# Optimization experiments

Hardware: AMD Instinct MI355X
Metric: run time of the kernel (lower is better)

The kernel has to match this reference:

```python
import jax, jax.numpy as jnp
import numpy as np
import math

BLOCK = 8
N_COEFF = BLOCK * BLOCK  # 64
N_SAMPLE = 250
SEED = 0  # args.seed

# zigzag order: flat index m*8+n from the hardcoded loc table
ZIGZAG = jnp.array([
    0, 1, 8, 16, 9, 2, 3, 10, 17, 24, 32, 25, 18, 11, 4, 5,
    12, 19, 26, 33, 40, 48, 41, 34, 27, 20, 13, 6, 7, 14, 21, 28,
    35, 42, 49, 56, 57, 50, 43, 36, 29, 22, 15, 23, 30, 37, 44, 51,
    58, 59, 52, 45, 38, 31, 39, 46, 53, 60, 61, 54, 47, 55, 62, 63
], dtype=jnp.int32)


def dct_matrix():
    Q = np.zeros((BLOCK, BLOCK), dtype=np.float32)
    Q[0, :] = math.sqrt(1.0 / BLOCK)
    for i in range(1, BLOCK):
        for j in range(BLOCK):
            Q[i, j] = math.sqrt(2.0 / BLOCK) * math.cos((2 * j + 1) * math.pi * i / (2.0 * BLOCK))
    return jnp.asarray(Q)


def setup_inputs() -> dict:
    key = jax.random.key(0)
    x = jax.random.uniform(key, (64, 3, 512, 512), dtype=jnp.float32)
    return {"x": x}


def reference(x):
    Q = dct_matrix()
    # rgb -> ycbcr, luminance channel only (module discards Cb/Cr)
    x255 = x * 255.0
    y = (0.299 * x255[:, 0] + 0.587 * x255[:, 1] + 0.114 * x255[:, 2]) / 255.0  # [B,H,W]
    B, H, W = y.shape
    a, b = H // BLOCK, W // BLOCK
    # split into 8x8 blocks: [B, a, b, 8, 8]
    blocks = y.reshape(B, a, BLOCK, b, BLOCK).transpose(0, 1, 3, 2, 4)
    # per-block 2D DCT: Q @ block @ Q^T, batched as one einsum
    dct = jnp.einsum('ij,nabjk,lk->nabil', Q, blocks, Q)  # [B,a,b,8,8]
    image_dct_result = dct.transpose(0, 1, 3, 2, 4).reshape(B, 1, H, W)
    # zigzag gather over flattened block coefficients -> [B, 64, a*b]
    dist = dct.reshape(B, a * b, N_COEFF)[:, :, ZIGZAG].transpose(0, 2, 1)
    # per (sample, coefficient) random permutation sampling of 250 blocks
    keys = jax.random.split(jax.random.key(SEED), B * N_COEFF)
    idx = jax.vmap(lambda k: jax.random.permutation(k, a * b)[:N_SAMPLE])(keys)
    idx = idx.reshape(B, N_COEFF, N_SAMPLE)
    dct_coeff_sample = jnp.take_along_axis(dist, idx, axis=2)  # [B,64,250]
    return image_dct_result, dct_coeff_sample
```

## Files before the change

kernel.cpp:

```cpp
#include <hip/hip_runtime.h>
#include <hip/hip_bf16.h>
#include <cstdint>


#define BATCH 64
#define HW 512
#define NBLK 4096
#define NSAMPLE 250
#define IMG_ELEMS (HW * HW)

#define A0 0.35355339059327373f
#define A1 0.49039264020161522f
#define A2 0.46193976625564337f
#define A3 0.41573480615127262f
#define A4 0.35355339059327379f
#define A5 0.27778511650980111f
#define A6 0.19134171618254492f
#define A7 0.09754516100806412f

__constant__ float Qc[8][8] = {
    { A0,  A0,  A0,  A0,  A0,  A0,  A0,  A0},
    { A1,  A3,  A5,  A7, -A7, -A5, -A3, -A1},
    { A2,  A6, -A6, -A2, -A2, -A6,  A6,  A2},
    { A3, -A7, -A1, -A5,  A5,  A1,  A7, -A3},
    { A4, -A4, -A4,  A4,  A4, -A4, -A4,  A4},
    { A5, -A1,  A7,  A3, -A3, -A7,  A1, -A5},
    { A6, -A2,  A2, -A6, -A6,  A2, -A2,  A6},
    { A7, -A5,  A3, -A1,  A1, -A3,  A5, -A7},
};

__constant__ int ZIGZAG[64] = {
    0, 1, 8, 16, 9, 2, 3, 10, 17, 24, 32, 25, 18, 11, 4, 5,
    12, 19, 26, 33, 40, 48, 41, 34, 27, 20, 13, 6, 7, 14, 21, 28,
    35, 42, 49, 56, 57, 50, 43, 36, 29, 22, 15, 23, 30, 37, 44, 51,
    58, 59, 52, 45, 38, 31, 39, 46, 53, 60, 61, 54, 47, 55, 62, 63
};

__device__ __forceinline__ uint32_t rotl32(uint32_t v, int d) {
    return (v << d) | (v >> (32 - d));
}

__device__ __forceinline__ void tf2x32(uint32_t k0, uint32_t k1,
                                       uint32_t x0, uint32_t x1,
                                       uint32_t& o0, uint32_t& o1) {
    uint32_t ks0 = k0, ks1 = k1, ks2 = k0 ^ k1 ^ 0x1BD11BDAu;
    x0 += ks0; x1 += ks1;
#define TF_R(r) { x0 += x1; x1 = rotl32(x1, r); x1 ^= x0; }
    TF_R(13) TF_R(15) TF_R(26) TF_R(6)
    x0 += ks1; x1 += ks2 + 1u;
    TF_R(17) TF_R(29) TF_R(16) TF_R(24)
    x0 += ks2; x1 += ks0 + 2u;
    TF_R(13) TF_R(15) TF_R(26) TF_R(6)
    x0 += ks0; x1 += ks1 + 3u;
    TF_R(17) TF_R(29) TF_R(16) TF_R(24)
    x0 += ks1; x1 += ks2 + 4u;
    TF_R(13) TF_R(15) TF_R(26) TF_R(6)
    x0 += ks2; x1 += ks0 + 5u;
#undef TF_R
    o0 = x0; o1 = x1;
}

__device__ __forceinline__ void build4096(
    uint32_t s0, uint32_t s1,
    uint32_t* __restrict__ pack32, uint32_t* __restrict__ hist,
    int tid, int w, int lane, uint32_t* __restrict__ wsum) {

    __syncthreads();
    ((uint4*)hist)[tid] = make_uint4(0u, 0u, 0u, 0u);
    ((uint4*)hist)[tid + 512] = make_uint4(0u, 0u, 0u, 0u);
    uint32_t keys[8];
#pragma unroll
    for (int e = 0; e < 8; ++e) {
        uint32_t o0, o1;
        tf2x32(s0, s1, 0u, (uint32_t)(tid + e * 512), o0, o1);
        keys[e] = o0 ^ o1;
    }
    __syncthreads();

    uint32_t ord[8];
#pragma unroll
    for (int e = 0; e < 8; ++e)
        ord[e] = atomicAdd(&hist[keys[e] >> 20], 1u);
    __syncthreads();

    uint4 va = ((const uint4*)hist)[tid * 2];
    uint4 vb = ((const uint4*)hist)[tid * 2 + 1];
    uint32_t ssum = va.x + va.y + va.z + va.w + vb.x + vb.y + vb.z + vb.w;
    uint32_t sc = ssum;
#pragma unroll
    for (int off = 1; off < 64; off <<= 1) {
        uint32_t t = __shfl_up(sc, off);
        if (lane >= off) sc += t;
    }
    if (lane == 63) wsum[w] = sc;
    __syncthreads();
    uint32_t ex = sc - ssum;
    for (int ww = 0; ww < w; ++ww) ex += wsum[ww];
    uint32_t p1 = ex + va.x, p2 = p1 + va.y, p3 = p2 + va.z, p4 = p3 + va.w;
    uint32_t p5 = p4 + vb.x, p6 = p5 + vb.y, p7 = p6 + vb.z, p8 = p7 + vb.w;
    ((uint4*)hist)[tid * 2] = make_uint4(p1, p2, p3, p4);
    ((uint4*)hist)[tid * 2 + 1] = make_uint4(p5, p6, p7, p8);
    __syncthreads();

#pragma unroll
    for (int e = 0; e < 8; ++e) {
        uint32_t bkt = keys[e] >> 20;
        uint32_t start = bkt ? hist[bkt - 1] : 0u;
        pack32[start + ord[e]] =
            ((keys[e] & 0xFFFFFu) << 12) | (uint32_t)(tid + e * 512);
    }
}

__device__ __forceinline__ uint32_t select4096(
    const uint32_t* __restrict__ hist, const uint32_t* __restrict__ pack32,
    uint32_t s) {
    uint32_t lo = 0, hi = 4095;
#pragma unroll
    for (int it = 0; it < 12; ++it) {
        uint32_t mid = (lo + hi) >> 1;
        if (hist[mid] > s) hi = mid; else lo = mid + 1;
    }
    uint32_t b = lo;
    uint32_t start = b ? hist[b - 1] : 0u;
    uint32_t L = hist[b] - start;
    uint32_t c = pack32[start];
    if (L > 1) {
        uint32_t k = s - start;
        for (uint32_t cand = 0; cand < L; ++cand) {
            uint32_t cc = pack32[start + cand];
            uint32_t cnt = 0;
            for (uint32_t o = 0; o < L; ++o)
                cnt += (pack32[start + o] < cc) ? 1u : 0u;
            if (cnt == k) { c = cc; break; }
        }
    }
    return c & 0xFFFu;
}

__global__ __launch_bounds__(512, 8) void fused_kernel(
    const float* __restrict__ x, float* __restrict__ out,
    uint32_t* __restrict__ ws) {
    __shared__ __align__(16) uint8_t smem[33280];
    __shared__ uint32_t wsum[8];

    const int tid = threadIdx.x;
    const int gb = blockIdx.x;

    {
        float* ylds = (float*)smem;
        const int b = gb >> 6;
        const int ai = gb & 63;
        const int row0 = ai * 8;
        const int h = tid >> 8;
        const int t2 = tid & 255;
        const int colbase = h * 256;

        {
            const int k = t2 >> 5;
            const int cg = t2 & 31;
            size_t off = (size_t)b * 3 * IMG_ELEMS + (size_t)(row0 + k) * HW +
                         colbase + cg * 8;
            float4 r0 = *(const float4*)(x + off);
            float4 r1 = *(const float4*)(x + off + 4);
            float4 g0 = *(const float4*)(x + off + IMG_ELEMS);
            float4 g1 = *(const float4*)(x + off + IMG_ELEMS + 4);
            float4 b0 = *(const float4*)(x + off + 2 * IMG_ELEMS);
            float4 b1 = *(const float4*)(x + off + 2 * IMG_ELEMS + 4);
            float R[8] = {r0.x, r0.y, r0.z, r0.w, r1.x, r1.y, r1.z, r1.w};
            float G[8] = {g0.x, g0.y, g0.z, g0.w, g1.x, g1.y, g1.z, g1.w};
            float B[8] = {b0.x, b0.y, b0.z, b0.w, b1.x, b1.y, b1.z, b1.w};
            float* yh = ylds + h * 2048 + k * 256;
#pragma unroll
            for (int jj = 0; jj < 8; ++jj) {
                float y = (0.299f * (R[jj] * 255.0f) + 0.587f * (G[jj] * 255.0f) +
                           0.114f * (B[jj] * 255.0f)) / 255.0f;
                yh[jj * 32 + cg] = y;
            }
        }
        __syncthreads();

        {
            const int i = t2 >> 5;
            const int bi = t2 & 31;
            const float* yh = ylds + h * 2048;
            float qrow[8];
#pragma unroll
            for (int k = 0; k < 8; ++k) qrow[k] = Qc[i][k];

            float acc[8];
#pragma unroll
            for (int j = 0; j < 8; ++j) acc[j] = 0.0f;
#pragma unroll
            for (int k = 0; k < 8; ++k) {
#pragma unroll
                for (int j = 0; j < 8; ++j)
                    acc[j] += qrow[k] * yh[k * 256 + j * 32 + bi];
            }

            float d[8];
#pragma unroll
            for (int j = 0; j < 8; ++j) {
                float s = 0.0f;
#pragma unroll
                for (int k = 0; k < 8; ++k) s += acc[k] * Qc[j][k];
                d[j] = s;
            }
            float4* o = (float4*)(out + (size_t)b * IMG_ELEMS +
                                  (size_t)(row0 + i) * HW + colbase + bi * 8);
            o[0] = make_float4(d[0], d[1], d[2], d[3]);
            o[1] = make_float4(d[4], d[5], d[6], d[7]);
        }
    }

    {
        uint32_t* pack32 = (uint32_t*)smem;
        uint32_t* hist = (uint32_t*)(smem + 16384);
        uint16_t* jsel = (uint16_t*)(smem + 32768);

        const int w = tid >> 6;
        const int lane = tid & 63;

        uint32_t k0, k1, n0, n1, sA0, sA1, sB0, sB1;
        tf2x32(0u, 0u, 0u, (uint32_t)gb, k0, k1);
        tf2x32(k0, k1, 0u, 0u, n0, n1);
        tf2x32(k0, k1, 0u, 1u, sA0, sA1);
        tf2x32(n0, n1, 0u, 1u, sB0, sB1);

        build4096(sB0, sB1, pack32, hist, tid, w, lane, wsum);
        __syncthreads();
        if (tid < NSAMPLE)
            jsel[tid] = (uint16_t)select4096(hist, pack32, (uint32_t)tid);

        build4096(sA0, sA1, pack32, hist, tid, w, lane, wsum);
        __syncthreads();

        int b = gb >> 6, c = gb & 63;
        int z = ZIGZAG[c];
        int i0z = z >> 3, j0z = z & 7;
        if (tid < NSAMPLE) {
            uint32_t i = select4096(hist, pack32, (uint32_t)jsel[tid]);
            int ai = (int)i >> 6, bi = (int)i & 63;
            ws[(size_t)gb * 256 + tid] =
                (uint32_t)((size_t)b * IMG_ELEMS +
                           (size_t)(ai * 8 + i0z) * HW + (bi * 8 + j0z));
        }
    }
}

__global__ __launch_bounds__(256) void gather_kernel(
    const float* __restrict__ img, const uint32_t* __restrict__ ws,
    float* __restrict__ out2) {
    const int gb = blockIdx.x;
    const int s = threadIdx.x;
    if (s < NSAMPLE)
        out2[(size_t)gb * NSAMPLE + s] = img[ws[(size_t)gb * 256 + s]];
}

extern "C" void kernel_launch(void* const* d_in, const int* in_sizes, int n_in,
                              void* d_out, int out_size, void* d_ws, size_t ws_size,
                              hipStream_t stream) {
    const float* x = (const float*)d_in[0];
    float* out = (float*)d_out;
    uint32_t* ws = (uint32_t*)d_ws;
    fused_kernel<<<NBLK, 512, 0, stream>>>(x, out, ws);
    gather_kernel<<<BATCH * 64, 256, 0, stream>>>(
        out, ws, out + (size_t)BATCH * IMG_ELEMS);
}
```

Before: 359.7 us.

## Split DCT into two LDS-staged passes and rank first permutation directly

The DCT is restructured into a column pass that writes intermediate results to a second LDS region, then a row pass that reads them back. This cuts the per-thread arithmetic from the fused triple loop to two 8x8 matrix-vector products, at the cost of one extra barrier and extra LDS traffic. For the first permutation, only elements whose bucket start falls within the first 250 slots are scattered. Each of those threads computes its exact rank inside its bucket and writes jsel directly, replacing the per-sample binary search and the fallback tie-resolution loop.

New measurement: 359.1 us. No clear change (-0.2%).

```diff
diff --git a/kernel.cpp b/kernel.cpp
--- a/kernel.cpp
+++ b/kernel.cpp
@@ -60,15 +60,14 @@
     o0 = x0; o1 = x1;
 }
 
-__device__ __forceinline__ void build4096(
-    uint32_t s0, uint32_t s1,
-    uint32_t* __restrict__ pack32, uint32_t* __restrict__ hist,
-    int tid, int w, int lane, uint32_t* __restrict__ wsum) {
+__device__ __forceinline__ void build_common(
+    uint32_t s0, uint32_t s1, uint32_t* __restrict__ hist,
+    int tid, int w, int lane, uint32_t* __restrict__ wsum,
+    uint32_t keys[8], uint32_t ord[8]) {
 
     __syncthreads();
     ((uint4*)hist)[tid] = make_uint4(0u, 0u, 0u, 0u);
     ((uint4*)hist)[tid + 512] = make_uint4(0u, 0u, 0u, 0u);
-    uint32_t keys[8];
 #pragma unroll
     for (int e = 0; e < 8; ++e) {
         uint32_t o0, o1;
@@ -77,7 +76,6 @@
     }
     __syncthreads();
 
-    uint32_t ord[8];
 #pragma unroll
     for (int e = 0; e < 8; ++e)
         ord[e] = atomicAdd(&hist[keys[e] >> 20], 1u);
@@ -101,14 +99,6 @@
     ((uint4*)hist)[tid * 2] = make_uint4(p1, p2, p3, p4);
     ((uint4*)hist)[tid * 2 + 1] = make_uint4(p5, p6, p7, p8);
     __syncthreads();
-
-#pragma unroll
-    for (int e = 0; e < 8; ++e) {
-        uint32_t bkt = keys[e] >> 20;
-        uint32_t start = bkt ? hist[bkt - 1] : 0u;
-        pack32[start + ord[e]] =
-            ((keys[e] & 0xFFFFFu) << 12) | (uint32_t)(tid + e * 512);
-    }
 }
 
 __device__ __forceinline__ uint32_t select4096(
@@ -147,13 +137,14 @@
     const int gb = blockIdx.x;
 
     {
-        float* ylds = (float*)smem;
         const int b = gb >> 6;
         const int ai = gb & 63;
         const int row0 = ai * 8;
         const int h = tid >> 8;
         const int t2 = tid & 255;
         const int colbase = h * 256;
+        float* ybase = (float*)smem + h * 2048;
+        float* ubase = (float*)(smem + 16384) + h * 2048;
 
         {
             const int k = t2 >> 5;
@@ -169,7 +160,7 @@
             float R[8] = {r0.x, r0.y, r0.z, r0.w, r1.x, r1.y, r1.z, r1.w};
             float G[8] = {g0.x, g0.y, g0.z, g0.w, g1.x, g1.y, g1.z, g1.w};
             float B[8] = {b0.x, b0.y, b0.z, b0.w, b1.x, b1.y, b1.z, b1.w};
-            float* yh = ylds + h * 2048 + k * 256;
+            float* yh = ybase + k * 256;
 #pragma unroll
             for (int jj = 0; jj < 8; ++jj) {
                 float y = (0.299f * (R[jj] * 255.0f) + 0.587f * (G[jj] * 255.0f) +
@@ -180,29 +171,39 @@
         __syncthreads();
 
         {
+            const int cp = t2 >> 5;
+            const int bi = t2 & 31;
+            float y[8];
+#pragma unroll
+            for (int k = 0; k < 8; ++k)
+                y[k] = ybase[k * 256 + cp * 32 + bi];
+            float u[8];
+#pragma unroll
+            for (int i = 0; i < 8; ++i) {
+                float s = 0.0f;
+#pragma unroll
+                for (int k = 0; k < 8; ++k) s += Qc[i][k] * y[k];
+                u[i] = s;
+            }
+#pragma unroll
+            for (int i = 0; i < 8; ++i)
+                ubase[i * 256 + cp * 32 + bi] = u[i];
+        }
+        __syncthreads();
+
+        {
             const int i = t2 >> 5;
             const int bi = t2 & 31;
-            const float* yh = ylds + h * 2048;
-            float qrow[8];
-#pragma unroll
-            for (int k = 0; k < 8; ++k) qrow[k] = Qc[i][k];
-
-            float acc[8];
-#pragma unroll
-            for (int j = 0; j < 8; ++j) acc[j] = 0.0f;
-#pragma unroll
-            for (int k = 0; k < 8; ++k) {
-#pragma unroll
-                for (int j = 0; j < 8; ++j)
-                    acc[j] += qrow[k] * yh[k * 256 + j * 32 + bi];
-            }
-
+            float qy[8];
+#pragma unroll
+            for (int c = 0; c < 8; ++c)
+                qy[c] = ubase[i * 256 + c * 32 + bi];
             float d[8];
 #pragma unroll
             for (int j = 0; j < 8; ++j) {
                 float s = 0.0f;
 #pragma unroll
-                for (int k = 0; k < 8; ++k) s += acc[k] * Qc[j][k];
+                for (int c = 0; c < 8; ++c) s += qy[c] * Qc[j][c];
                 d[j] = s;
             }
             float4* o = (float4*)(out + (size_t)b * IMG_ELEMS +
@@ -226,12 +227,41 @@
         tf2x32(k0, k1, 0u, 1u, sA0, sA1);
         tf2x32(n0, n1, 0u, 1u, sB0, sB1);
 
-        build4096(sB0, sB1, pack32, hist, tid, w, lane, wsum);
-        __syncthreads();
-        if (tid < NSAMPLE)
-            jsel[tid] = (uint16_t)select4096(hist, pack32, (uint32_t)tid);
-
-        build4096(sA0, sA1, pack32, hist, tid, w, lane, wsum);
+        uint32_t keys[8], ord[8];
+
+        build_common(sB0, sB1, hist, tid, w, lane, wsum, keys, ord);
+        uint32_t starts[8];
+#pragma unroll
+        for (int e = 0; e < 8; ++e) {
+            uint32_t bkt = keys[e] >> 20;
+            starts[e] = bkt ? hist[bkt - 1] : 0u;
+            if (starts[e] < NSAMPLE)
+                pack32[starts[e] + ord[e]] =
+                    ((keys[e] & 0xFFFFFu) << 12) | (uint32_t)(tid + e * 512);
+        }
+        __syncthreads();
+#pragma unroll
+        for (int e = 0; e < 8; ++e) {
+            if (starts[e] < NSAMPLE) {
+                uint32_t bkt = keys[e] >> 20;
+                uint32_t end = hist[bkt];
+                uint32_t self =
+                    ((keys[e] & 0xFFFFFu) << 12) | (uint32_t)(tid + e * 512);
+                uint32_t r = starts[e];
+                for (uint32_t p = starts[e]; p < end; ++p)
+                    r += (pack32[p] < self) ? 1u : 0u;
+                if (r < NSAMPLE) jsel[r] = (uint16_t)(tid + e * 512);
+            }
+        }
+
+        build_common(sA0, sA1, hist, tid, w, lane, wsum, keys, ord);
+#pragma unroll
+        for (int e = 0; e < 8; ++e) {
+            uint32_t bkt = keys[e] >> 20;
+            uint32_t start = bkt ? hist[bkt - 1] : 0u;
+            pack32[start + ord[e]] =
+                ((keys[e] & 0xFFFFFu) << 12) | (uint32_t)(tid + e * 512);
+        }
         __syncthreads();
 
         int b = gb >> 6, c = gb & 63;
```
